# Kernel optimization log

Measured on AMD Instinct MI355X. Metric: run time of the kernel, lower is better.

The kernel has to match this reference:

```python
import jax, jax.numpy as jnp
import numpy as np

EPS = 1e-5
NUM_HEADS = 16

def layernorm(x, g, b):
    mu = jnp.mean(x, axis=-1, keepdims=True)
    var = jnp.mean(jnp.square(x - mu), axis=-1, keepdims=True)
    return (x - mu) * jax.lax.rsqrt(var + EPS) * g + b

def setup_inputs() -> dict:
    key = jax.random.key(0)
    ks = jax.random.split(key, 5)
    B, N, C = 2, 2048, 1024
    s_in = 1.0 / np.sqrt(C)
    return {
        "x": jax.random.normal(ks[0], (B, N, C), jnp.float32),
        "ln1_g": jnp.ones((C,), jnp.float32),
        "ln1_b": jnp.zeros((C,), jnp.float32),
        "w_qk": jax.random.normal(ks[1], (C, 2 * C), jnp.float32) * s_in,
        "w_v": jax.random.normal(ks[2], (C, C), jnp.float32) * s_in,
        "ln2_g": jnp.ones((C,), jnp.float32),
        "ln2_b": jnp.zeros((C,), jnp.float32),
        "w_proj": jax.random.normal(ks[3], (C, C), jnp.float32) * s_in,
        "b_proj": jnp.zeros((C,), jnp.float32),
    }

def reference(x, ln1_g, ln1_b, w_qk, w_v, ln2_g, ln2_b, w_proj, b_proj):
    B, N, C = x.shape
    H = NUM_HEADS
    hd = C // H
    scale = hd ** (-0.5)
    xn = layernorm(x, ln1_g, ln1_b)
    # qk: [B,N,2C] -> q,k each [B,H,N,hd]
    qk = (xn @ w_qk).reshape(B, N, 2, H, hd).transpose(2, 0, 3, 1, 4)
    q, k = qk[0], qk[1]
    v = (xn @ w_v).reshape(B, N, H, hd).transpose(0, 2, 1, 3)  # [B,H,N,hd]
    attn = jnp.einsum("bhqd,bhkd->bhqk", q, k) * scale
    attn = jax.nn.softmax(attn, axis=-1)
    out = jnp.einsum("bhqk,bhkd->bhqd", attn, v)  # [B,H,N,hd]
    out = out.transpose(0, 2, 1, 3).reshape(B, N, C)
    out = layernorm(out, ln2_g, ln2_b)
    return out @ w_proj + b_proj
```

## Files before the change

kernel.cpp:

```cpp
#include <hip/hip_runtime.h>
#include <hip/hip_bf16.h>


typedef __attribute__((ext_vector_type(8))) short short8;
typedef __attribute__((ext_vector_type(4))) short short4v;
typedef __attribute__((ext_vector_type(4))) float float4v;

__device__ __forceinline__ unsigned short f2bf(float f) {
    unsigned u = __builtin_bit_cast(unsigned, f);
    return (unsigned short)((u + 0x7FFFu + ((u >> 16) & 1u)) >> 16);
}
__device__ __forceinline__ unsigned packbf2(float lo, float hi) {
    return __builtin_amdgcn_perm(__builtin_bit_cast(unsigned, hi) + 0x8000u,
                                 __builtin_bit_cast(unsigned, lo) + 0x8000u,
                                 0x07060302u);
}
__device__ __forceinline__ void gll16(const unsigned short* g, unsigned short* l) {
    __builtin_amdgcn_global_load_lds(
        (const __attribute__((address_space(1))) unsigned int*)g,
        (__attribute__((address_space(3))) unsigned int*)l, 16, 0, 0);
}

__global__ __launch_bounds__(256) void prep(
    const float* __restrict__ x, const float* __restrict__ g1, const float* __restrict__ b1,
    const float* __restrict__ w_qk, const float* __restrict__ w_v,
    const float* __restrict__ w_proj, const float* __restrict__ g2,
    const float* __restrict__ b2,
    unsigned short* __restrict__ xn, unsigned short* __restrict__ wqkvT,
    unsigned short* __restrict__ wgT, float* __restrict__ u, float* __restrict__ w0) {
    __shared__ float sh[32 * 33];
    const int bid = blockIdx.x, tid = threadIdx.x;
    if (bid < 4096) {
        const float4 v = reinterpret_cast<const float4*>(x + (size_t)bid * 1024)[tid];
        float s  = v.x + v.y + v.z + v.w;
        float sq = v.x * v.x + v.y * v.y + v.z * v.z + v.w * v.w;
#pragma unroll
        for (int off = 32; off >= 1; off >>= 1) {
            s  += __shfl_xor(s, off, 64);
            sq += __shfl_xor(sq, off, 64);
        }
        const int w = tid >> 6, lane = tid & 63;
        if (lane == 0) { sh[w] = s; sh[4 + w] = sq; }
        __syncthreads();
        s  = sh[0] + sh[1] + sh[2] + sh[3];
        sq = sh[4] + sh[5] + sh[6] + sh[7];
        const float mu = s * (1.f / 1024.f);
        const float rstd = rsqrtf(sq * (1.f / 1024.f) - mu * mu + 1e-5f);
        const float4 gv = reinterpret_cast<const float4*>(g1)[tid];
        const float4 bv = reinterpret_cast<const float4*>(b1)[tid];
        ushort4 o;
        o.x = f2bf((v.x - mu) * rstd * gv.x + bv.x);
        o.y = f2bf((v.y - mu) * rstd * gv.y + bv.y);
        o.z = f2bf((v.z - mu) * rstd * gv.z + bv.z);
        o.w = f2bf((v.w - mu) * rstd * gv.w + bv.w);
        *reinterpret_cast<ushort4*>(&xn[(size_t)bid * 1024 + tid * 4]) = o;
    } else {
        const float* in; unsigned short* out; int Cc, bx, by; bool doU = false;
        if (bid < 6144)      { int t = bid - 4096; in = w_qk;   out = wqkvT;               Cc = 2048; bx = t & 63; by = t >> 6; }
        else if (bid < 7168) { int t = bid - 6144; in = w_v;    out = wqkvT + 2048 * 1024; Cc = 1024; bx = t & 31; by = t >> 5; }
        else                 { int t = bid - 7168; in = w_proj; out = wgT; doU = true;     Cc = 1024; bx = t & 31; by = t >> 5; }
        const int c0 = bx * 32, r0 = by * 32;
        const int tx = tid & 31, ty = tid >> 5;
#pragma unroll
        for (int i = 0; i < 32; i += 8)
            sh[(ty + i) * 33 + tx] = in[(size_t)(r0 + ty + i) * Cc + c0 + tx];
        __syncthreads();
        const float scale = doU ? g2[r0 + tx] : 1.f;
        const float b2v   = doU ? b2[r0 + tx] : 0.f;
#pragma unroll
        for (int i = 0; i < 32; i += 8) {
            const float raw = sh[tx * 33 + ty + i];
            const float sc  = raw * scale;
            out[(size_t)(c0 + ty + i) * 1024 + r0 + tx] = f2bf(sc);
            if (doU) {
                float pu = sc, pw = raw * b2v;
#pragma unroll
                for (int off = 1; off <= 16; off <<= 1) {
                    pu += __shfl_xor(pu, off, 64);
                    pw += __shfl_xor(pw, off, 64);
                }
                if (tx == 0) {
                    atomicAdd(&u[c0 + ty + i], pu);
                    atomicAdd(&w0[c0 + ty + i], pw);
                }
            }
        }
    }
}

__global__ __launch_bounds__(512) void gemm256_qkv(const unsigned short* __restrict__ A,
                                                   const unsigned short* __restrict__ Bt,
                                                   unsigned short* __restrict__ qb,
                                                   unsigned short* __restrict__ kb,
                                                   unsigned short* __restrict__ vT) {
    __shared__ unsigned short As[2 * 256 * 64], Bs[2 * 256 * 64];
    const int tid = threadIdx.x, lane = tid & 63, w = tid >> 6;
    const int wm = (w >> 2) * 128, wn = (w & 3) * 64;
    const int quad = lane >> 4, l16 = lane & 15;
    const int ls = lane >> 3, sg = lane & 7;
    const int m0 = blockIdx.y * 256, n0 = blockIdx.x * 256;

    float4v acc[8][4];
#pragma unroll
    for (int mi = 0; mi < 8; mi++)
#pragma unroll
        for (int ni = 0; ni < 4; ni++) acc[mi][ni] = float4v{0.f, 0.f, 0.f, 0.f};

    const int g = (sg ^ ls) * 8;
#pragma unroll 1
    for (int s = -1; s < 16; s++) {
        if (s >= 0) __syncthreads();
        if (s + 1 < 16) {
            const int k0 = (s + 1) << 6, buf = ((s + 1) & 1) << 14;
            unsigned short* Ad = As + buf;
            unsigned short* Bd = Bs + buf;
#pragma unroll
            for (int i = 0; i < 4; i++) {
                const int r = w * 32 + i * 8 + ls;
                gll16(&A[(size_t)(m0 + r) * 1024 + k0 + g], &Ad[(w * 32 + i * 8) * 64]);
                gll16(&Bt[(size_t)(n0 + r) * 1024 + k0 + g], &Bd[(w * 32 + i * 8) * 64]);
            }
        }
        if (s < 0) continue;
        const unsigned short* Ac = As + ((s & 1) << 14);
        const unsigned short* Bc = Bs + ((s & 1) << 14);
#pragma unroll
        for (int ks = 0; ks < 2; ks++) {
            short8 af[8], bfr[4];
#pragma unroll
            for (int mi = 0; mi < 8; mi++) {
                const int r = wm + mi * 16 + l16;
                af[mi] = *reinterpret_cast<const short8*>(
                    &Ac[r * 64 + ((ks * 4 + quad) ^ (r & 7)) * 8]);
            }
#pragma unroll
            for (int ni = 0; ni < 4; ni++) {
                const int r = wn + ni * 16 + l16;
                bfr[ni] = *reinterpret_cast<const short8*>(
                    &Bc[r * 64 + ((ks * 4 + quad) ^ (r & 7)) * 8]);
            }
#pragma unroll
            for (int mi = 0; mi < 8; mi++)
#pragma unroll
                for (int ni = 0; ni < 4; ni++)
                    acc[mi][ni] = __builtin_amdgcn_mfma_f32_16x16x32_bf16(
                        af[mi], bfr[ni], acc[mi][ni], 0, 0, 0);
        }
    }

    const float QSCALE = 0.125f * 1.4426950408889634f;
#pragma unroll
    for (int mi = 0; mi < 8; mi++) {
        const int row0 = m0 + wm + mi * 16 + quad * 4;
        const int b = row0 >> 11, nq = row0 & 2047;
#pragma unroll
        for (int ni = 0; ni < 4; ni++) {
            const int col = n0 + wn + ni * 16 + l16;
            if (col < 1024) {
                const int h = col >> 6, d = col & 63;
#pragma unroll
                for (int r = 0; r < 4; r++)
                    qb[(((size_t)b * 16 + h) * 2048 + nq + r) * 64 + d] =
                        f2bf(acc[mi][ni][r] * QSCALE);
            } else if (col < 2048) {
                const int c = col - 1024, h = c >> 6, d = c & 63;
#pragma unroll
                for (int r = 0; r < 4; r++)
                    kb[(((size_t)b * 16 + h) * 2048 + nq + r) * 64 + d] = f2bf(acc[mi][ni][r]);
            } else {
                const int c = col - 2048, h = c >> 6, d = c & 63;
                const short4v sv = {(short)f2bf(acc[mi][ni][0]), (short)f2bf(acc[mi][ni][1]),
                                    (short)f2bf(acc[mi][ni][2]), (short)f2bf(acc[mi][ni][3])};
                *reinterpret_cast<short4v*>(
                    &vT[(((size_t)b * 16 + h) * 64 + d) * 2048 + nq]) = sv;
            }
        }
    }
}

__global__ __launch_bounds__(512) void flash_attn(const unsigned short* __restrict__ qbuf,
                                                  const unsigned short* __restrict__ kb,
                                                  const unsigned short* __restrict__ vT,
                                                  unsigned short* __restrict__ attn,
                                                  float2* __restrict__ part) {
    __shared__ unsigned short Ks[2][64 * 64];
    __shared__ unsigned short Vs[2][64 * 64];
    const int tid = threadIdx.x, lane = tid & 63, w = tid >> 6;
    const int quad = lane >> 4, l16 = lane & 15;
    const int ls = lane >> 3, sg = lane & 7;
    const int qt = blockIdx.x, bh = blockIdx.y;
    const int q0 = qt * 256;
    const size_t nbase = (size_t)bh * 2048;

    short8 bq[2][2];
#pragma unroll
    for (int q2 = 0; q2 < 2; q2++)
#pragma unroll
        for (int ks = 0; ks < 2; ks++)
            bq[q2][ks] = *reinterpret_cast<const short8*>(
                &qbuf[(nbase + q0 + w * 32 + q2 * 16 + l16) * 64 + ks * 32 + quad * 8]);

    float l_part[2] = {0.f, 0.f};
    float4v o_acc[2][4];
#pragma unroll
    for (int q2 = 0; q2 < 2; q2++)
#pragma unroll
        for (int db = 0; db < 4; db++) o_acc[q2][db] = float4v{0.f, 0.f, 0.f, 0.f};

    const int vd = tid >> 3, vG0 = (tid & 7) * 2;
#pragma unroll 1
    for (int s = -1; s < 32; s++) {
        if (s >= 0) __syncthreads();
        if (s + 1 < 32) {
            const int kt0 = (s + 1) << 6, buf = (s + 1) & 1;
            gll16(&kb[(nbase + kt0 + w * 8 + ls) * 64 + ((sg ^ ls) << 3)],
                  &Ks[buf][(w * 8) * 64]);
            const uint4 vv = *reinterpret_cast<const uint4*>(
                &vT[((size_t)bh * 64 + vd) * 2048 + kt0 + (vG0 << 2)]);
            *reinterpret_cast<short4v*>(&Vs[buf][(vd << 6) + ((vG0 ^ (vd & 15)) << 2)]) =
                __builtin_bit_cast(short4v, uint2{vv.x, vv.y});
            *reinterpret_cast<short4v*>(&Vs[buf][(vd << 6) + (((vG0 + 1) ^ (vd & 15)) << 2)]) =
                __builtin_bit_cast(short4v, uint2{vv.z, vv.w});
        }
        if (s < 0) continue;
        const unsigned short* Kc = Ks[s & 1];
        const unsigned short* Vc = Vs[s & 1];

        short8 kf[2][4];
#pragma unroll
        for (int ks = 0; ks < 2; ks++)
#pragma unroll
            for (int cb = 0; cb < 4; cb++) {
                const int r = cb * 16 + l16;
                kf[ks][cb] = *reinterpret_cast<const short8*>(
                    &Kc[r * 64 + ((ks * 4 + quad) ^ (r & 7)) * 8]);
            }
        short4v vb[4][4];
#pragma unroll
        for (int kt = 0; kt < 4; kt++)
#pragma unroll
            for (int db = 0; db < 4; db++)
                vb[kt][db] = *reinterpret_cast<const short4v*>(
                    &Vc[((db * 16 + l16) << 6) + (((kt * 4 + quad) ^ l16) << 2)]);

#pragma unroll
        for (int q2 = 0; q2 < 2; q2++) {
            float4v s_acc[4];
#pragma unroll
            for (int cb = 0; cb < 4; cb++) s_acc[cb] = float4v{0.f, 0.f, 0.f, 0.f};
#pragma unroll
            for (int ks = 0; ks < 2; ks++)
#pragma unroll
                for (int cb = 0; cb < 4; cb++)
                    s_acc[cb] = __builtin_amdgcn_mfma_f32_16x16x32_bf16(
                        kf[ks][cb], bq[q2][ks], s_acc[cb], 0, 0, 0);

            short4v pa[4];
            float ls2 = 0.f;
#pragma unroll
            for (int cb = 0; cb < 4; cb++) {
                const float p0 = __builtin_amdgcn_exp2f(s_acc[cb][0]);
                const float p1 = __builtin_amdgcn_exp2f(s_acc[cb][1]);
                const float p2 = __builtin_amdgcn_exp2f(s_acc[cb][2]);
                const float p3 = __builtin_amdgcn_exp2f(s_acc[cb][3]);
                ls2 += (p0 + p1) + (p2 + p3);
                pa[cb] = __builtin_bit_cast(short4v,
                          uint2{packbf2(p0, p1), packbf2(p2, p3)});
            }
            l_part[q2] += ls2;
#pragma unroll
            for (int kt = 0; kt < 4; kt++)
#pragma unroll
                for (int db = 0; db < 4; db++)
                    o_acc[q2][db] = __builtin_amdgcn_mfma_f32_16x16x16bf16_1k(
                        pa[kt], vb[kt][db], o_acc[q2][db], 0, 0, 0);
        }
    }

    const int b = bh >> 4, h = bh & 15;
#pragma unroll
    for (int q2 = 0; q2 < 2; q2++) {
        float lr = l_part[q2];
        lr += __shfl_xor(lr, 16, 64);
        lr += __shfl_xor(lr, 32, 64);
#pragma unroll
        for (int r = 0; r < 4; r++) {
            const float lq = __shfl(lr, quad * 4 + r, 64);
            const float inv = 1.f / lq;
            const int rowl = q0 + w * 32 + q2 * 16 + quad * 4 + r;
            const int grow = b * 2048 + rowl;
            float s = 0.f, s2 = 0.f;
#pragma unroll
            for (int db = 0; db < 4; db++) {
                const float on = o_acc[q2][db][r] * inv;
                attn[(size_t)grow * 1024 + h * 64 + db * 16 + l16] = f2bf(on);
                s += on;
                s2 = fmaf(on, on, s2);
            }
#pragma unroll
            for (int off = 1; off <= 8; off <<= 1) {
                s  += __shfl_xor(s, off, 64);
                s2 += __shfl_xor(s2, off, 64);
            }
            if (l16 == 0) part[(size_t)grow * 16 + h] = float2{s, s2};
        }
    }
}

__device__ __forceinline__ void stage_tiles(const unsigned short* __restrict__ A,
                                            const unsigned short* __restrict__ Bt,
                                            int K, int m0, int n0, int k0,
                                            unsigned short* As, unsigned short* Bs,
                                            int w, int ls, int sg) {
#pragma unroll
    for (int i = 0; i < 4; i++) {
        const int r = w * 32 + i * 8 + ls;
        const int g = (sg ^ ls) * 8;
        gll16(&A[(size_t)(m0 + r) * K + k0 + g], &As[(w * 32 + i * 8) * 64]);
        gll16(&Bt[(size_t)(n0 + r) * K + k0 + g], &Bs[(w * 32 + i * 8) * 64]);
    }
}

__device__ __forceinline__ void gemm128_core(const unsigned short* __restrict__ A,
                                             const unsigned short* __restrict__ Bt,
                                             int K, int m0, int n0,
                                             unsigned short* As, unsigned short* Bs,
                                             float4v acc[4][4]) {
    const int tid = threadIdx.x, lane = tid & 63, w = tid >> 6;
    const int wr = (w >> 1) * 64, wc = (w & 1) * 64;
    const int quad = lane >> 4, l16 = lane & 15;
    const int ls = lane >> 3, sg = lane & 7;
#pragma unroll
    for (int mi = 0; mi < 4; mi++)
#pragma unroll
        for (int ni = 0; ni < 4; ni++) acc[mi][ni] = float4v{0.f, 0.f, 0.f, 0.f};

    const int NS = K >> 6;
    stage_tiles(A, Bt, K, m0, n0, 0, As, Bs, w, ls, sg);
    for (int s = 0; s < NS; s++) {
        __syncthreads();
        const int cur = (s & 1) << 13;
        if (s + 1 < NS)
            stage_tiles(A, Bt, K, m0, n0, (s + 1) << 6,
                        As + (((s + 1) & 1) << 13), Bs + (((s + 1) & 1) << 13),
                        w, ls, sg);
        const unsigned short* Ac = As + cur;
        const unsigned short* Bc = Bs + cur;
#pragma unroll
        for (int ks = 0; ks < 2; ks++) {
            short8 af[4], bfr[4];
#pragma unroll
            for (int mi = 0; mi < 4; mi++) {
                const int r = wr + mi * 16 + l16;
                af[mi] = *reinterpret_cast<const short8*>(
                    &Ac[r * 64 + ((ks * 4 + quad) ^ (r & 7)) * 8]);
            }
#pragma unroll
            for (int ni = 0; ni < 4; ni++) {
                const int r = wc + ni * 16 + l16;
                bfr[ni] = *reinterpret_cast<const short8*>(
                    &Bc[r * 64 + ((ks * 4 + quad) ^ (r & 7)) * 8]);
            }
#pragma unroll
            for (int mi = 0; mi < 4; mi++)
#pragma unroll
                for (int ni = 0; ni < 4; ni++)
                    acc[mi][ni] = __builtin_amdgcn_mfma_f32_16x16x32_bf16(
                        af[mi], bfr[ni], acc[mi][ni], 0, 0, 0);
        }
    }
}

__global__ __launch_bounds__(256) void gemm128_proj(const unsigned short* __restrict__ A,
                                                    const unsigned short* __restrict__ Bt,
                                                    const float2* __restrict__ part,
                                                    const float* __restrict__ u,
                                                    const float* __restrict__ w0,
                                                    const float* __restrict__ bias,
                                                    float* __restrict__ out) {
    __shared__ unsigned short As[2 * 128 * 64], Bs[2 * 128 * 64];
    __shared__ float2 rstat_s[128];
    const int m0 = blockIdx.y * 128, n0 = blockIdx.x * 128;
    {
        const int t = threadIdx.x, rloc = t >> 1, half = t & 1;
        const float4* p4 = reinterpret_cast<const float4*>(part);
        float s = 0.f, s2 = 0.f;
#pragma unroll
        for (int j = 0; j < 4; j++) {
            const float4 p = p4[(size_t)(m0 + rloc) * 8 + half * 4 + j];
            s += p.x + p.z; s2 += p.y + p.w;
        }
        s  += __shfl_xor(s, 1, 64);
        s2 += __shfl_xor(s2, 1, 64);
        if (!half) {
            const float mu = s * (1.f / 1024.f);
            const float rstd = rsqrtf(s2 * (1.f / 1024.f) - mu * mu + 1e-5f);
            rstat_s[rloc] = float2{rstd, mu * rstd};
        }
    }
    float4v acc[4][4];
    gemm128_core(A, Bt, 1024, m0, n0, As, Bs, acc);
    const int lane = threadIdx.x & 63, w = threadIdx.x >> 6;
    const int wr = (w >> 1) * 64, wc = (w & 1) * 64;
    const int quad = lane >> 4, l16 = lane & 15;
#pragma unroll
    for (int mi = 0; mi < 4; mi++) {
        const int rl0 = wr + mi * 16 + quad * 4;
        float2 rs[4];
#pragma unroll
        for (int r = 0; r < 4; r++) rs[r] = rstat_s[rl0 + r];
#pragma unroll
        for (int ni = 0; ni < 4; ni++) {
            const int col = n0 + wc + ni * 16 + l16;
            const float uu = u[col], ww = w0[col] + bias[col];
#pragma unroll
            for (int r = 0; r < 4; r++)
                out[(size_t)(m0 + rl0 + r) * 1024 + col] =
                    fmaf(rs[r].x, acc[mi][ni][r], ww - rs[r].y * uu);
        }
    }
}

extern "C" void kernel_launch(void* const* d_in, const int* in_sizes, int n_in,
                              void* d_out, int out_size, void* d_ws, size_t ws_size,
                              hipStream_t stream) {
    const float* x      = (const float*)d_in[0];
    const float* ln1_g  = (const float*)d_in[1];
    const float* ln1_b  = (const float*)d_in[2];
    const float* w_qk   = (const float*)d_in[3];
    const float* w_v    = (const float*)d_in[4];
    const float* ln2_g  = (const float*)d_in[5];
    const float* ln2_b  = (const float*)d_in[6];
    const float* w_proj = (const float*)d_in[7];
    const float* b_proj = (const float*)d_in[8];
    float* out = (float*)d_out;

    char* ws = (char*)d_ws;
    unsigned short* xn      = (unsigned short*)(ws + 0);
    unsigned short* wqkvT   = (unsigned short*)(ws + 8388608);
    unsigned short* wgT     = (unsigned short*)(ws + 14680064);
    unsigned short* qbuf    = (unsigned short*)(ws + 16777216);
    unsigned short* kbuf    = (unsigned short*)(ws + 25165824);
    unsigned short* vTbuf   = (unsigned short*)(ws + 33554432);
    unsigned short* attn    = (unsigned short*)(ws + 41943040);
    float2*         part    = (float2*)(ws + 50331648);
    float*          u       = (float*)(ws + 50888704);
    float*          w0      = (float*)(ws + 50892800);

    hipMemsetAsync(ws + 50888704, 0, 8192, stream);
    prep<<<8192, 256, 0, stream>>>(x, ln1_g, ln1_b, w_qk, w_v, w_proj, ln2_g, ln2_b,
                                   xn, wqkvT, wgT, u, w0);
    gemm256_qkv<<<dim3(12, 16), 512, 0, stream>>>(xn, wqkvT, qbuf, kbuf, vTbuf);
    flash_attn<<<dim3(8, 32), 512, 0, stream>>>(qbuf, kbuf, vTbuf, attn, part);
    gemm128_proj<<<dim3(8, 32), 256, 0, stream>>>(attn, wgT, part, u, w0, b_proj, out);
}
```

Baseline: 221.1 us.

## Restructure flash attention: direct V loads, 16x16x32 PV MFMA, smaller blocks

The flash-attention kernel stops staging V through shared memory. Each wave now reads V fragments straight from global memory and runs the P·V product with the 16x16x32 bf16 MFMA, packing P into 8-wide operands. K rows are loaded into LDS in a permuted order so the score layout matches the new P operand layout. Blocks shrink to 256 threads over 128 queries, which doubles the grid, and the epilogue writes 4-wide vectors with fewer shuffles. The cost is redundant global V reads across waves and more blocks re-reading K.

```diff
diff --git a/kernel.cpp b/kernel.cpp
--- a/kernel.cpp
+++ b/kernel.cpp
@@ -5,6 +5,7 @@
 typedef __attribute__((ext_vector_type(8))) short short8;
 typedef __attribute__((ext_vector_type(4))) short short4v;
 typedef __attribute__((ext_vector_type(4))) float float4v;
+typedef __attribute__((ext_vector_type(4))) unsigned uint4v;
 
 __device__ __forceinline__ unsigned short f2bf(float f) {
     unsigned u = __builtin_bit_cast(unsigned, f);
@@ -178,19 +179,25 @@
     }
 }
 
-__global__ __launch_bounds__(512) void flash_attn(const unsigned short* __restrict__ qbuf,
+__global__ __launch_bounds__(256) void flash_attn(const unsigned short* __restrict__ qbuf,
                                                   const unsigned short* __restrict__ kb,
                                                   const unsigned short* __restrict__ vT,
                                                   unsigned short* __restrict__ attn,
                                                   float2* __restrict__ part) {
     __shared__ unsigned short Ks[2][64 * 64];
-    __shared__ unsigned short Vs[2][64 * 64];
     const int tid = threadIdx.x, lane = tid & 63, w = tid >> 6;
     const int quad = lane >> 4, l16 = lane & 15;
     const int ls = lane >> 3, sg = lane & 7;
-    const int qt = blockIdx.x, bh = blockIdx.y;
-    const int q0 = qt * 256;
+    const int q0 = blockIdx.x * 128, bh = blockIdx.y;
     const size_t nbase = (size_t)bh * 2048;
+
+    int srow[2];
+#pragma unroll
+    for (int i = 0; i < 2; i++) {
+        const int pr = w * 16 + i * 8 + ls;
+        srow[i] = (pr & 32) | ((pr & 12) << 1) | ((pr & 16) >> 2) | (pr & 3);
+    }
+    const int sgran = (sg ^ ls) << 3;
 
     short8 bq[2][2];
 #pragma unroll
@@ -207,25 +214,30 @@
 #pragma unroll
         for (int db = 0; db < 4; db++) o_acc[q2][db] = float4v{0.f, 0.f, 0.f, 0.f};
 
-    const int vd = tid >> 3, vG0 = (tid & 7) * 2;
+#pragma unroll
+    for (int i = 0; i < 2; i++)
+        gll16(&kb[(nbase + srow[i]) * 64 + sgran], &Ks[0][(w * 16 + i * 8) * 64]);
+
 #pragma unroll 1
-    for (int s = -1; s < 32; s++) {
-        if (s >= 0) __syncthreads();
+    for (int s = 0; s < 32; s++) {
+        const int kt0 = s << 6;
+        __syncthreads();
         if (s + 1 < 32) {
-            const int kt0 = (s + 1) << 6, buf = (s + 1) & 1;
-            gll16(&kb[(nbase + kt0 + w * 8 + ls) * 64 + ((sg ^ ls) << 3)],
-                  &Ks[buf][(w * 8) * 64]);
-            const uint4 vv = *reinterpret_cast<const uint4*>(
-                &vT[((size_t)bh * 64 + vd) * 2048 + kt0 + (vG0 << 2)]);
-            *reinterpret_cast<short4v*>(&Vs[buf][(vd << 6) + ((vG0 ^ (vd & 15)) << 2)]) =
-                __builtin_bit_cast(short4v, uint2{vv.x, vv.y});
-            *reinterpret_cast<short4v*>(&Vs[buf][(vd << 6) + (((vG0 + 1) ^ (vd & 15)) << 2)]) =
-                __builtin_bit_cast(short4v, uint2{vv.z, vv.w});
-        }
-        if (s < 0) continue;
+            const int ktn = (s + 1) << 6;
+#pragma unroll
+            for (int i = 0; i < 2; i++)
+                gll16(&kb[(nbase + ktn + srow[i]) * 64 + sgran],
+                      &Ks[(s + 1) & 1][(w * 16 + i * 8) * 64]);
+        }
+        short8 va[2][4];
+#pragma unroll
+        for (int k2 = 0; k2 < 2; k2++)
+#pragma unroll
+            for (int db = 0; db < 4; db++)
+                va[k2][db] = *reinterpret_cast<const short8*>(
+                    &vT[((size_t)bh * 64 + db * 16 + l16) * 2048 + kt0 + k2 * 32 + quad * 8]);
+
         const unsigned short* Kc = Ks[s & 1];
-        const unsigned short* Vc = Vs[s & 1];
-
         short8 kf[2][4];
 #pragma unroll
         for (int ks = 0; ks < 2; ks++)
@@ -235,13 +247,6 @@
                 kf[ks][cb] = *reinterpret_cast<const short8*>(
                     &Kc[r * 64 + ((ks * 4 + quad) ^ (r & 7)) * 8]);
             }
-        short4v vb[4][4];
-#pragma unroll
-        for (int kt = 0; kt < 4; kt++)
-#pragma unroll
-            for (int db = 0; db < 4; db++)
-                vb[kt][db] = *reinterpret_cast<const short4v*>(
-                    &Vc[((db * 16 + l16) << 6) + (((kt * 4 + quad) ^ l16) << 2)]);
 
 #pragma unroll
         for (int q2 = 0; q2 < 2; q2++) {
@@ -255,25 +260,31 @@
                     s_acc[cb] = __builtin_amdgcn_mfma_f32_16x16x32_bf16(
                         kf[ks][cb], bq[q2][ks], s_acc[cb], 0, 0, 0);
 
-            short4v pa[4];
             float ls2 = 0.f;
-#pragma unroll
-            for (int cb = 0; cb < 4; cb++) {
-                const float p0 = __builtin_amdgcn_exp2f(s_acc[cb][0]);
-                const float p1 = __builtin_amdgcn_exp2f(s_acc[cb][1]);
-                const float p2 = __builtin_amdgcn_exp2f(s_acc[cb][2]);
-                const float p3 = __builtin_amdgcn_exp2f(s_acc[cb][3]);
-                ls2 += (p0 + p1) + (p2 + p3);
-                pa[cb] = __builtin_bit_cast(short4v,
-                          uint2{packbf2(p0, p1), packbf2(p2, p3)});
+            short8 pb[2];
+#pragma unroll
+            for (int k2 = 0; k2 < 2; k2++) {
+                float p[8];
+#pragma unroll
+                for (int cc = 0; cc < 2; cc++)
+#pragma unroll
+                    for (int r = 0; r < 4; r++) {
+                        const float pv = __builtin_amdgcn_exp2f(s_acc[k2 * 2 + cc][r]);
+                        p[cc * 4 + r] = pv;
+                        ls2 += pv;
+                    }
+                uint4v pd;
+                pd.x = packbf2(p[0], p[1]); pd.y = packbf2(p[2], p[3]);
+                pd.z = packbf2(p[4], p[5]); pd.w = packbf2(p[6], p[7]);
+                pb[k2] = __builtin_bit_cast(short8, pd);
             }
             l_part[q2] += ls2;
 #pragma unroll
-            for (int kt = 0; kt < 4; kt++)
+            for (int k2 = 0; k2 < 2; k2++)
 #pragma unroll
                 for (int db = 0; db < 4; db++)
-                    o_acc[q2][db] = __builtin_amdgcn_mfma_f32_16x16x16bf16_1k(
-                        pa[kt], vb[kt][db], o_acc[q2][db], 0, 0, 0);
+                    o_acc[q2][db] = __builtin_amdgcn_mfma_f32_16x16x32_bf16(
+                        va[k2][db], pb[k2], o_acc[q2][db], 0, 0, 0);
         }
     }
 
@@ -283,27 +294,22 @@
         float lr = l_part[q2];
         lr += __shfl_xor(lr, 16, 64);
         lr += __shfl_xor(lr, 32, 64);
-#pragma unroll
-        for (int r = 0; r < 4; r++) {
-            const float lq = __shfl(lr, quad * 4 + r, 64);
-            const float inv = 1.f / lq;
-            const int rowl = q0 + w * 32 + q2 * 16 + quad * 4 + r;
-            const int grow = b * 2048 + rowl;
-            float s = 0.f, s2 = 0.f;
-#pragma unroll
-            for (int db = 0; db < 4; db++) {
-                const float on = o_acc[q2][db][r] * inv;
-                attn[(size_t)grow * 1024 + h * 64 + db * 16 + l16] = f2bf(on);
-                s += on;
-                s2 = fmaf(on, on, s2);
-            }
-#pragma unroll
-            for (int off = 1; off <= 8; off <<= 1) {
-                s  += __shfl_xor(s, off, 64);
-                s2 += __shfl_xor(s2, off, 64);
-            }
-            if (l16 == 0) part[(size_t)grow * 16 + h] = float2{s, s2};
-        }
+        const float inv = 1.f / lr;
+        const int grow = b * 2048 + q0 + w * 32 + q2 * 16 + l16;
+        float s = 0.f, s2 = 0.f;
+#pragma unroll
+        for (int db = 0; db < 4; db++) {
+            const float o0 = o_acc[q2][db][0] * inv, o1 = o_acc[q2][db][1] * inv;
+            const float o2 = o_acc[q2][db][2] * inv, o3 = o_acc[q2][db][3] * inv;
+            const ushort4 st = {f2bf(o0), f2bf(o1), f2bf(o2), f2bf(o3)};
+            *reinterpret_cast<ushort4*>(
+                &attn[(size_t)grow * 1024 + h * 64 + db * 16 + quad * 4]) = st;
+            s  += (o0 + o1) + (o2 + o3);
+            s2 += (o0 * o0 + o1 * o1) + (o2 * o2 + o3 * o3);
+        }
+        s  += __shfl_xor(s, 16, 64);  s  += __shfl_xor(s, 32, 64);
+        s2 += __shfl_xor(s2, 16, 64); s2 += __shfl_xor(s2, 32, 64);
+        if (quad == 0) part[(size_t)grow * 16 + h] = float2{s, s2};
     }
 }
 
@@ -451,6 +457,6 @@
     prep<<<8192, 256, 0, stream>>>(x, ln1_g, ln1_b, w_qk, w_v, w_proj, ln2_g, ln2_b,
                                    xn, wqkvT, wgT, u, w0);
     gemm256_qkv<<<dim3(12, 16), 512, 0, stream>>>(xn, wqkvT, qbuf, kbuf, vTbuf);
-    flash_attn<<<dim3(8, 32), 512, 0, stream>>>(qbuf, kbuf, vTbuf, attn, part);
+    flash_attn<<<dim3(16, 32), 256, 0, stream>>>(qbuf, kbuf, vTbuf, attn, part);
     gemm128_proj<<<dim3(8, 32), 256, 0, stream>>>(attn, wgT, part, u, w0, b_proj, out);
 }
```

Result: slower. 230.0 us (+4.0%).
